# Optimization experiments

Measured on AMD Instinct MI355X. Metric: run time of the kernel, lower is better.

## Reference

```python
import jax, jax.numpy as jnp
import numpy as np

DIM = 64
HID = 64      # hidden_dim
BATCH = 16384


def setup_inputs() -> dict:
    key = jax.random.key(0)
    ks = jax.random.split(key, 11)
    s = 0.05
    x = jax.random.normal(ks[0], (BATCH, DIM), dtype=jnp.float32)
    # network 0: Linear(1,H) -> ReLU -> Linear(H,2)
    w0 = jax.random.normal(ks[1], (1, HID), dtype=jnp.float32) * s
    b0 = jax.random.normal(ks[2], (HID,), dtype=jnp.float32) * s
    v0 = jax.random.normal(ks[3], (HID, 2), dtype=jnp.float32) * s
    c0 = jax.random.normal(ks[4], (2,), dtype=jnp.float32) * s
    # networks 1..DIM-1: Linear(i,H) -> ReLU -> Linear(H,H) -> ReLU -> Linear(H,2)
    # first-layer weights padded to full width DIM; columns >= i are masked out in reference().
    W1 = jax.random.normal(ks[5], (DIM - 1, DIM, HID), dtype=jnp.float32) * s
    B1 = jax.random.normal(ks[6], (DIM - 1, HID), dtype=jnp.float32) * s
    W2 = jax.random.normal(ks[7], (DIM - 1, HID, HID), dtype=jnp.float32) * s
    B2 = jax.random.normal(ks[8], (DIM - 1, HID), dtype=jnp.float32) * s
    W3 = jax.random.normal(ks[9], (DIM - 1, HID, 2), dtype=jnp.float32) * s
    B3 = jax.random.normal(ks[10], (DIM - 1, 2), dtype=jnp.float32) * s
    return {"x": x, "w0": w0, "b0": b0, "v0": v0, "c0": c0,
            "W1": W1, "B1": B1, "W2": W2, "B2": B2, "W3": W3, "B3": B3}


def reference(x, w0, b0, v0, c0, W1, B1, W2, B2, W3, B3):
    B, dim = x.shape
    # mask[i, j] = 1 if j < (i+1): network i+1 sees x[:, :i+1] prefix of width i+1... actually width i+1? No:
    # network index k (k = 1..dim-1) sees x[:, :k]. Row i of the stacks corresponds to k = i+1,
    # so valid input columns are j < i+1.
    mask = (jnp.arange(dim)[None, :] <= jnpp_dummy) if False else (jnp.arange(dim)[None, :] < (jnp.arange(1, dim)[:, None]))
    mask = mask.astype(x.dtype)                      # [dim-1, dim]
    W1m = W1 * mask[:, :, None]                      # zero out padded input columns
    h1 = jax.nn.relu(jnp.einsum('bd,idh->bih', x, W1m) + B1)   # [B, dim-1, H]
    h2 = jax.nn.relu(jnp.einsum('bih,ihg->big', h1, W2) + B2)  # [B, dim-1, H]
    out = jnp.einsum('big,igo->bio', h2, W3) + B3               # [B, dim-1, 2]
    # network 0 receives a constant ones input -> output is constant across the batch
    h0 = jax.nn.relu(w0[0] + b0)                     # [H]
    out0 = h0 @ v0 + c0                              # [2]
    out0 = jnp.broadcast_to(out0[None, None, :], (B, 1, 2))
    full = jnp.concatenate([out0, out], axis=1)      # [B, dim, 2]
    scales = jnp.clip(full[..., 0], -5.0, 5.0)
    translations = full[..., 1]
    return scales, translations

jnp_dummy = None
```

## Files before the change

### kernel.cpp

```cpp
#include <hip/hip_runtime.h>
#include <hip/hip_bf16.h>

#define BATCH 16384

typedef __attribute__((ext_vector_type(8))) short short8;
typedef __attribute__((ext_vector_type(4))) short short4v;
typedef __attribute__((ext_vector_type(2))) short sshort2;
typedef __attribute__((ext_vector_type(8))) unsigned short ushort8;
typedef __attribute__((ext_vector_type(4))) unsigned short ushort4v;
typedef __attribute__((ext_vector_type(4))) float float4v;

#define FR_STRIDE  18944u
#define FR_SIZE    (63u * FR_STRIDE)
#define OFF_A2     8192u
#define OFF_A3     16384u
#define OFF_B1     18432u
#define OFF_B2     18688u
#define XBF_SIZE   2097152u
#define FR_ELEMS   1184

__device__ __forceinline__ unsigned int packbf2(float a, float b) {
#if __has_builtin(__builtin_amdgcn_cvt_pk_bf16_f32)
    typedef __attribute__((ext_vector_type(2))) __bf16 bf2_t;
    union { bf2_t h; unsigned int u; } v;
    v.h = __builtin_amdgcn_cvt_pk_bf16_f32(a, b);
    return v.u;
#else
    union { __hip_bfloat162 h; unsigned int u; } v;
    v.h = __float22bfloat162_rn(make_float2(a, b));
    return v.u;
#endif
}
__device__ __forceinline__ unsigned int relu_pk(unsigned int u) {
#if __has_builtin(__builtin_elementwise_max)
    union { sshort2 s; unsigned int w; } v; v.w = u;
    v.s = __builtin_elementwise_max(v.s, (sshort2)0);
    return v.w;
#else
    unsigned int lo = (u & 0x8000u) ? 0u : (u & 0xFFFFu);
    unsigned int hi = (u & 0x80000000u) ? 0u : (u & 0xFFFF0000u);
    return lo | hi;
#endif
}
__device__ __forceinline__ unsigned int cvt_relu(float a, float b) {
    return relu_pk(packbf2(a, b));
}
__device__ __forceinline__ unsigned short f2bf(float a) {
    union { __hip_bfloat16 h; unsigned short u; } v;
    v.h = __float2bfloat16(a);
    return v.u;
}

__device__ __forceinline__ void gl_lds16(const char* gsrc, char* ldst) {
    __builtin_amdgcn_global_load_lds(
        (const __attribute__((address_space(1))) unsigned int*)gsrc,
        (__attribute__((address_space(3))) unsigned int*)ldst,
        16, 0, 0);
}

__global__ __launch_bounds__(256) void setup_kernel(
    const float* __restrict__ x,
    const float* __restrict__ W1,
    const float* __restrict__ W2,
    const float* __restrict__ W3,
    const float* __restrict__ B1,
    const float* __restrict__ B2,
    char* __restrict__ frag,
    char* __restrict__ xbf)
{
    const int b = blockIdx.x;
    const int t = threadIdx.x;

    if (b >= 63) {
        const int idx = (b - 63) * 256 + t;
        const float* xp = x + (size_t)idx * 16;
        char* dst = xbf + (size_t)idx * 32;
        #pragma unroll
        for (int h = 0; h < 2; ++h) {
            float4v f0 = *(const float4v*)(xp + h * 8);
            float4v f1 = *(const float4v*)(xp + h * 8 + 4);
            union { ushort8 s; unsigned int u[4]; } p;
            p.u[0] = packbf2(f0[0], f0[1]);
            p.u[1] = packbf2(f0[2], f0[3]);
            p.u[2] = packbf2(f1[0], f1[1]);
            p.u[3] = packbf2(f1[2], f1[3]);
            *(ushort8*)(dst + h * 16) = p.s;
        }
        return;
    }

    __shared__ float sW1[4096];
    __shared__ float sW2[4096];

    const int kn   = b;
    const int net  = kn + 1;
    const int lane = t & 63;
    const int grp  = t >> 6;
    const int lq   = lane & 15;
    const int quad = lane >> 4;

    {
        const float4v* s1 = (const float4v*)(W1 + kn * 4096);
        const float4v* s2 = (const float4v*)(W2 + kn * 4096);
        #pragma unroll
        for (int i = 0; i < 4; ++i) {
            ((float4v*)sW1)[i * 256 + t] = s1[i * 256 + t];
            ((float4v*)sW2)[i * 256 + t] = s2[i * 256 + t];
        }
    }
    __syncthreads();

    char* base = frag + (size_t)kn * FR_STRIDE;

    {
        const int h = lq + 16 * grp;
        ushort8 a10, a11;
        #pragma unroll
        for (int j = 0; j < 8; ++j) {
            const int d0 = quad * 8 + j;
            const int d1 = d0 + 32;
            a10[j] = (d0 < net) ? f2bf(sW1[d0 * 64 + h]) : (unsigned short)0;
            a11[j] = (d1 < net) ? f2bf(sW1[d1 * 64 + h]) : (unsigned short)0;
        }
        char* dst = base + grp * 2048 + lane * 32;
        *(ushort8*)(dst)      = a10;
        *(ushort8*)(dst + 16) = a11;
    }

    {
        const int g = lq + 16 * grp;
        #pragma unroll
        for (int p = 0; p < 2; ++p) {
            ushort8 v;
            #pragma unroll
            for (int j = 0; j < 8; ++j) {
                const int h = 32 * p + ((j & 4) << 2) + 4 * quad + (j & 3);
                v[j] = f2bf(sW2[h * 64 + g]);
            }
            *(ushort8*)(base + OFF_A2 + p * 4096 + grp * 1024 + lane * 16) = v;
        }
    }

    if (grp < 2) {
        const int p = grp;
        ushort8 v;
        #pragma unroll
        for (int j = 0; j < 8; ++j) {
            const int gg = 32 * p + ((j & 4) << 2) + 4 * quad + (j & 3);
            v[j] = (lq < 2) ? f2bf(W3[kn * 128 + gg * 2 + lq]) : (unsigned short)0;
        }
        *(ushort8*)(base + OFF_A3 + p * 1024 + lane * 16) = v;
    }

    if (t < 64) {
        *(float*)(base + OFF_B1 + t * 4) = B1[kn * 64 + t];
        *(float*)(base + OFF_B2 + t * 4) = B2[kn * 64 + t];
    }
}

template <bool XBF>
__global__ __launch_bounds__(256, 3) void arnet_main4(
    const float* __restrict__ x,
    const char* __restrict__ xbf,
    const char* __restrict__ frag,
    const float* __restrict__ w0, const float* __restrict__ b0,
    const float* __restrict__ v0, const float* __restrict__ c0,
    const float* __restrict__ B3,
    float* __restrict__ out)
{
    const int bi    = blockIdx.x;
    const int chunk = bi & 63;
    const int gi    = bi >> 6;
    const int start = (gi < 8) ? 6 * gi : 48 + 4 * (gi - 8);
    const int cnt   = (gi < 8) ? 6 : 4;
    const int t     = threadIdx.x;

    const int lane = t & 63;
    const int w    = t >> 6;
    const int lq   = lane & 15;
    const int quad = lane >> 4;

    __shared__ __align__(16) char sFrag[2][FR_STRIDE];
    __shared__ float sOut[2][256][7];

    const int rowbase = chunk * 256 + w * 64;

    short8 xf[4][2];
    #pragma unroll
    for (int tm = 0; tm < 4; ++tm) {
        if (XBF) {
            const char* base = xbf + (size_t)(rowbase + 16 * tm + lq) * 128 + quad * 16;
            xf[tm][0] = *(const short8*)(base);
            xf[tm][1] = *(const short8*)(base + 64);
        } else {
            const float* xr = x + (size_t)(rowbase + 16 * tm + lq) * 64 + quad * 8;
            #pragma unroll
            for (int half = 0; half < 2; ++half) {
                float4v f0 = *(const float4v*)(xr + 32 * half);
                float4v f1 = *(const float4v*)(xr + 32 * half + 4);
                union { short8 s; unsigned int u[4]; } p;
                p.u[0] = packbf2(f0[0], f0[1]);
                p.u[1] = packbf2(f0[2], f0[3]);
                p.u[2] = packbf2(f1[0], f1[1]);
                p.u[3] = packbf2(f1[2], f1[3]);
                xf[tm][half] = p.s;
            }
        }
    }

    auto stage = [&](int net_, char* dstb) {
        const char* src = frag + (size_t)(net_ - 1) * FR_STRIDE;
        #pragma unroll
        for (int i = 0; i < 5; ++i) {
            const int e = i * 256 + t;
            if (e < FR_ELEMS)
                gl_lds16(src + e * 16, dstb + e * 16);
        }
    };

    const int first = (start == 0) ? 1 : 0;
    stage(start + first, sFrag[first & 1]);
    __syncthreads();

    #pragma unroll 1
    for (int idx = 0; idx < cnt; ++idx) {
        const int net = start + idx;

        if (idx + 1 < cnt && idx + 1 > first)
            stage(start + idx + 1, sFrag[(idx + 1) & 1]);

        if (net == 0) {
            float s = 0.f, tr = 0.f;
            #pragma unroll 8
            for (int j = 0; j < 64; ++j) {
                float h = fmaxf(w0[j] + b0[j], 0.f);
                s  += h * v0[2 * j];
                tr += h * v0[2 * j + 1];
            }
            s += c0[0];
            tr += c0[1];
            s = fminf(fmaxf(s, -5.f), 5.f);
            sOut[0][t][0] = s;
            sOut[1][t][0] = tr;
            __syncthreads();
            continue;
        }

        const int kn = net - 1;
        const char* sf  = sFrag[idx & 1];
        const char* pA1 = sf + lane * 32;
        const char* pA2 = sf + OFF_A2 + lane * 16;
        const char* pA3 = sf + OFF_A3 + lane * 16;
        const float* bB1 = (const float*)(sf + OFF_B1);
        const float* bB2 = (const float*)(sf + OFF_B2);

        const bool hiK = (net > 32);
        float4v acc2[4][4];
        #pragma unroll
        for (int p = 0; p < 2; ++p) {
            unsigned int pk[2][2][4];
            #pragma unroll
            for (int s = 0; s < 2; ++s) {
                const int th = 2 * p + s;
                short8 a10 = *(const short8*)(pA1 + th * 2048);
                float4v bias1 = *(const float4v*)(bB1 + quad * 4 + 16 * th);
                if (hiK) {
                    short8 a11 = *(const short8*)(pA1 + th * 2048 + 16);
                    #pragma unroll
                    for (int tm = 0; tm < 4; ++tm) {
                        float4v acc1;
                        acc1 = __builtin_amdgcn_mfma_f32_16x16x32_bf16(a10, xf[tm][0], bias1, 0, 0, 0);
                        acc1 = __builtin_amdgcn_mfma_f32_16x16x32_bf16(a11, xf[tm][1], acc1, 0, 0, 0);
                        pk[s][0][tm] = cvt_relu(acc1[0], acc1[1]);
                        pk[s][1][tm] = cvt_relu(acc1[2], acc1[3]);
                    }
                } else {
                    #pragma unroll
                    for (int tm = 0; tm < 4; ++tm) {
                        float4v acc1;
                        acc1 = __builtin_amdgcn_mfma_f32_16x16x32_bf16(a10, xf[tm][0], bias1, 0, 0, 0);
                        pk[s][0][tm] = cvt_relu(acc1[0], acc1[1]);
                        pk[s][1][tm] = cvt_relu(acc1[2], acc1[3]);
                    }
                }
            }
            #pragma unroll
            for (int tg = 0; tg < 4; ++tg) {
                short8 a2 = *(const short8*)(pA2 + p * 4096 + tg * 1024);
                float4v bias2 = *(const float4v*)(bB2 + quad * 4 + 16 * tg);
                #pragma unroll
                for (int tm = 0; tm < 4; ++tm) {
                    union { short8 s8; unsigned int u[4]; } bb;
                    bb.u[0] = pk[0][0][tm]; bb.u[1] = pk[0][1][tm];
                    bb.u[2] = pk[1][0][tm]; bb.u[3] = pk[1][1][tm];
                    acc2[tg][tm] = __builtin_amdgcn_mfma_f32_16x16x32_bf16(
                        a2, bb.s8, (p == 0) ? bias2 : acc2[tg][tm], 0, 0, 0);
                }
            }
        }

        float4v c3v;
        c3v[0] = B3[kn * 2]; c3v[1] = B3[kn * 2 + 1]; c3v[2] = 0.f; c3v[3] = 0.f;
        float4v acc3[4];
        #pragma unroll
        for (int p = 0; p < 2; ++p) {
            short8 a3 = *(const short8*)(pA3 + p * 1024);
            #pragma unroll
            for (int tm = 0; tm < 4; ++tm) {
                union { short8 s8; unsigned int u[4]; } bb;
                bb.u[0] = cvt_relu(acc2[2 * p][tm][0],     acc2[2 * p][tm][1]);
                bb.u[1] = cvt_relu(acc2[2 * p][tm][2],     acc2[2 * p][tm][3]);
                bb.u[2] = cvt_relu(acc2[2 * p + 1][tm][0], acc2[2 * p + 1][tm][1]);
                bb.u[3] = cvt_relu(acc2[2 * p + 1][tm][2], acc2[2 * p + 1][tm][3]);
                acc3[tm] = __builtin_amdgcn_mfma_f32_16x16x32_bf16(
                    a3, bb.s8, (p == 0) ? c3v : acc3[tm], 0, 0, 0);
            }
        }

        if (quad == 0) {
            #pragma unroll
            for (int tm = 0; tm < 4; ++tm) {
                const int lr = w * 64 + 16 * tm + lq;
                sOut[0][lr][idx] = fminf(fmaxf(acc3[tm][0], -5.f), 5.f);
                sOut[1][lr][idx] = acc3[tm][1];
            }
        }
        __syncthreads();
    }

    {
        const int row = t;
        const size_t grow = (size_t)chunk * 256 + row;
        #pragma unroll
        for (int o = 0; o < 2; ++o) {
            float* dst = out + ((size_t)o * BATCH + grow) * 64 + start;
            #pragma unroll
            for (int c = 0; c < 6; c += 2) {
                if (c < cnt) {
                    float2 v2;
                    v2.x = sOut[o][row][c];
                    v2.y = sOut[o][row][c + 1];
                    *(float2*)(dst + c) = v2;
                }
            }
        }
    }
}

#define WPAD 72
__global__ __launch_bounds__(256) void arnet_fallback(
    const float* __restrict__ x, const float* __restrict__ w0, const float* __restrict__ b0,
    const float* __restrict__ v0, const float* __restrict__ c0,
    const float* __restrict__ W1, const float* __restrict__ B1,
    const float* __restrict__ W2, const float* __restrict__ B2,
    const float* __restrict__ W3, const float* __restrict__ B3,
    float* __restrict__ out)
{
    const int bi = blockIdx.x;
    const int net = bi >> 5;
    const int tile = bi & 31;
    const int t = threadIdx.x;
    if (net == 0) {
        float s = 0.f, tr = 0.f;
        for (int j = 0; j < 64; ++j) {
            float h = fmaxf(w0[j] + b0[j], 0.f);
            s += h * v0[2 * j]; tr += h * v0[2 * j + 1];
        }
        s += c0[0]; tr += c0[1];
        s = fminf(fmaxf(s, -5.f), 5.f);
        const size_t r0 = (size_t)tile * 512;
        out[(r0 + t) * 64] = s; out[(size_t)BATCH * 64 + (r0 + t) * 64] = tr;
        out[(r0 + 256 + t) * 64] = s; out[(size_t)BATCH * 64 + (r0 + 256 + t) * 64] = tr;
        return;
    }
    __shared__ unsigned short sW1T[64 * WPAD];
    __shared__ unsigned short sW2T[64 * WPAD];
    __shared__ unsigned short sW3T[2 * 64];
    __shared__ float sB1[64];
    __shared__ float sB2[64];
    const int kn = net - 1;
    {
        const int hb = (t & 15) * 4, jb = (t >> 4) * 4;
        const float* src1 = W1 + kn * 4096;
        const float* src2 = W2 + kn * 4096;
        float4v a[4], b[4];
        for (int jj = 0; jj < 4; ++jj) {
            a[jj] = *(const float4v*)(src1 + (jb + jj) * 64 + hb);
            if (jb + jj >= net) a[jj] = (float4v)0.f;
            b[jj] = *(const float4v*)(src2 + (jb + jj) * 64 + hb);
        }
        for (int hh = 0; hh < 4; ++hh) {
            ushort4v ra, rb;
            for (int jj = 0; jj < 4; ++jj) { ra[jj] = f2bf(a[jj][hh]); rb[jj] = f2bf(b[jj][hh]); }
            *(ushort4v*)(&sW1T[(hb + hh) * WPAD + jb]) = ra;
            *(ushort4v*)(&sW2T[(hb + hh) * WPAD + jb]) = rb;
        }
    }
    if (t < 64) {
        sW3T[t] = f2bf(W3[kn * 128 + t * 2]);
        sW3T[64 + t] = f2bf(W3[kn * 128 + t * 2 + 1]);
        sB1[t] = B1[kn * 64 + t];
        sB2[t] = B2[kn * 64 + t];
    }
    const float b30 = B3[kn * 2], b31 = B3[kn * 2 + 1];
    __syncthreads();
    const int lane = t & 63, w = t >> 6, lq = lane & 15, quad = lane >> 4;
    for (int pass = 0; pass < 2; ++pass) {
        const int rowbase = tile * 512 + pass * 256 + w * 64;
        short8 xf[4][2];
        for (int tm = 0; tm < 4; ++tm) {
            const float* xr = x + (size_t)(rowbase + 16 * tm + lq) * 64 + quad * 8;
            for (int half = 0; half < 2; ++half) {
                float4v f0 = *(const float4v*)(xr + 32 * half);
                float4v f1 = *(const float4v*)(xr + 32 * half + 4);
                union { short8 s; unsigned int u[4]; } p;
                p.u[0] = packbf2(f0[0], f0[1]); p.u[1] = packbf2(f0[2], f0[3]);
                p.u[2] = packbf2(f1[0], f1[1]); p.u[3] = packbf2(f1[2], f1[3]);
                xf[tm][half] = p.s;
            }
        }
        float4v acc2[4][4];
        for (int tg = 0; tg < 4; ++tg) {
            float4v bias2 = *(const float4v*)(&sB2[quad * 4 + 16 * tg]);
            for (int tm = 0; tm < 4; ++tm) acc2[tg][tm] = bias2;
        }
        for (int th = 0; th < 4; ++th) {
            float4v bias1 = *(const float4v*)(&sB1[quad * 4 + 16 * th]);
            short8 a10 = *(const short8*)(&sW1T[(lq + 16 * th) * WPAD + quad * 8]);
            short8 a11 = *(const short8*)(&sW1T[(lq + 16 * th) * WPAD + quad * 8 + 32]);
            float4v acc1[4];
            for (int tm = 0; tm < 4; ++tm) {
                acc1[tm] = bias1;
                acc1[tm] = __builtin_amdgcn_mfma_f32_16x16x32_bf16(a10, xf[tm][0], acc1[tm], 0, 0, 0);
                acc1[tm] = __builtin_amdgcn_mfma_f32_16x16x32_bf16(a11, xf[tm][1], acc1[tm], 0, 0, 0);
            }
            short4v bf1[4];
            for (int tm = 0; tm < 4; ++tm) {
                union { short4v s; unsigned int u[2]; } pk;
                pk.u[0] = cvt_relu(acc1[tm][0], acc1[tm][1]);
                pk.u[1] = cvt_relu(acc1[tm][2], acc1[tm][3]);
                bf1[tm] = pk.s;
            }
            for (int tg = 0; tg < 4; ++tg) {
                short4v a2 = *(const short4v*)(&sW2T[(lq + 16 * tg) * WPAD + quad * 4 + 16 * th]);
                for (int tm = 0; tm < 4; ++tm)
                    acc2[tg][tm] = __builtin_amdgcn_mfma_f32_16x16x16bf16_1k(a2, bf1[tm], acc2[tg][tm], 0, 0, 0);
            }
        }
        float4v acc3[4];
        for (int tm = 0; tm < 4; ++tm) { acc3[tm][0] = b30; acc3[tm][1] = b31; acc3[tm][2] = 0.f; acc3[tm][3] = 0.f; }
        for (int tg = 0; tg < 4; ++tg) {
            short4v a3 = (short4v)0;
            if (lq < 2) a3 = *(const short4v*)(&sW3T[lq * 64 + quad * 4 + 16 * tg]);
            for (int tm = 0; tm < 4; ++tm) {
                union { short4v s; unsigned int u[2]; } pk;
                pk.u[0] = cvt_relu(acc2[tg][tm][0], acc2[tg][tm][1]);
                pk.u[1] = cvt_relu(acc2[tg][tm][2], acc2[tg][tm][3]);
                acc3[tm] = __builtin_amdgcn_mfma_f32_16x16x16bf16_1k(a3, pk.s, acc3[tm], 0, 0, 0);
            }
        }
        if (quad == 0) {
            for (int tm = 0; tm < 4; ++tm) {
                const size_t r = (size_t)(rowbase + 16 * tm + lq);
                out[r * 64 + net] = fminf(fmaxf(acc3[tm][0], -5.f), 5.f);
                out[(size_t)BATCH * 64 + r * 64 + net] = acc3[tm][1];
            }
        }
    }
}

extern "C" void kernel_launch(void* const* d_in, const int* in_sizes, int n_in,
                              void* d_out, int out_size, void* d_ws, size_t ws_size,
                              hipStream_t stream) {
    const float* x  = (const float*)d_in[0];
    const float* w0 = (const float*)d_in[1];
    const float* b0 = (const float*)d_in[2];
    const float* v0 = (const float*)d_in[3];
    const float* c0 = (const float*)d_in[4];
    const float* W1 = (const float*)d_in[5];
    const float* B1 = (const float*)d_in[6];
    const float* W2 = (const float*)d_in[7];
    const float* B2 = (const float*)d_in[8];
    const float* W3 = (const float*)d_in[9];
    const float* B3 = (const float*)d_in[10];
    float* out = (float*)d_out;
    char* ws = (char*)d_ws;

    const dim3 blk(256);

    if (ws_size >= FR_SIZE + XBF_SIZE) {
        char* xbf = ws + FR_SIZE;
        setup_kernel<<<dim3(63 + 256), blk, 0, stream>>>(x, W1, W2, W3, B1, B2, ws, xbf);
        arnet_main4<true><<<dim3(768), blk, 0, stream>>>(
            x, xbf, ws, w0, b0, v0, c0, B3, out);
    } else if (ws_size >= FR_SIZE) {
        setup_kernel<<<dim3(63), blk, 0, stream>>>(x, W1, W2, W3, B1, B2, ws, nullptr);
        arnet_main4<false><<<dim3(768), blk, 0, stream>>>(
            x, nullptr, ws, w0, b0, v0, c0, B3, out);
    } else {
        arnet_fallback<<<dim3(64 * 32), blk, 0, stream>>>(
            x, w0, b0, v0, c0, W1, B1, W2, B2, W3, B3, out);
    }
}
```

Before: 102.4 us.

## Balance per-block network assignment via pair table and raise MFMA wave priority

```diff
diff --git a/kernel.cpp b/kernel.cpp
--- a/kernel.cpp
+++ b/kernel.cpp
@@ -18,6 +18,12 @@
 #define OFF_B2     18688u
 #define XBF_SIZE   2097152u
 #define FR_ELEMS   1184
+
+__device__ const unsigned char PAIR_TBL[12][3] = {
+    {0, 1, 24}, {2, 3, 25}, {4, 5, 26}, {6, 7, 27},
+    {8, 9, 28}, {10, 11, 29}, {12, 13, 30}, {14, 15, 16},
+    {17, 18, 0}, {19, 20, 0}, {21, 22, 0}, {23, 31, 0}
+};
 
 __device__ __forceinline__ unsigned int packbf2(float a, float b) {
 #if __has_builtin(__builtin_amdgcn_cvt_pk_bf16_f32)
@@ -171,8 +177,8 @@
     const int bi    = blockIdx.x;
     const int chunk = bi & 63;
     const int gi    = bi >> 6;
-    const int start = (gi < 8) ? 6 * gi : 48 + 4 * (gi - 8);
-    const int cnt   = (gi < 8) ? 6 : 4;
+    const int npair = (gi < 8) ? 3 : 2;
+    const int cnt   = 2 * npair;
     const int t     = threadIdx.x;
 
     const int lane = t & 63;
@@ -184,6 +190,10 @@
     __shared__ float sOut[2][256][7];
 
     const int rowbase = chunk * 256 + w * 64;
+
+    auto netof = [&](int i) -> int {
+        return 2 * (int)PAIR_TBL[gi][i >> 1] + (i & 1);
+    };
 
     short8 xf[4][2];
     #pragma unroll
@@ -218,16 +228,16 @@
         }
     };
 
-    const int first = (start == 0) ? 1 : 0;
-    stage(start + first, sFrag[first & 1]);
+    const int first = (gi == 0) ? 1 : 0;
+    stage(netof(first), sFrag[first & 1]);
     __syncthreads();
 
     #pragma unroll 1
     for (int idx = 0; idx < cnt; ++idx) {
-        const int net = start + idx;
+        const int net = netof(idx);
 
         if (idx + 1 < cnt && idx + 1 > first)
-            stage(start + idx + 1, sFrag[(idx + 1) & 1]);
+            stage(netof(idx + 1), sFrag[(idx + 1) & 1]);
 
         if (net == 0) {
             float s = 0.f, tr = 0.f;
@@ -284,6 +294,7 @@
                     }
                 }
             }
+            __builtin_amdgcn_s_setprio(1);
             #pragma unroll
             for (int tg = 0; tg < 4; ++tg) {
                 short8 a2 = *(const short8*)(pA2 + p * 4096 + tg * 1024);
@@ -297,11 +308,13 @@
                         a2, bb.s8, (p == 0) ? bias2 : acc2[tg][tm], 0, 0, 0);
                 }
             }
+            __builtin_amdgcn_s_setprio(0);
         }
 
         float4v c3v;
         c3v[0] = B3[kn * 2]; c3v[1] = B3[kn * 2 + 1]; c3v[2] = 0.f; c3v[3] = 0.f;
         float4v acc3[4];
+        __builtin_amdgcn_s_setprio(1);
         #pragma unroll
         for (int p = 0; p < 2; ++p) {
             short8 a3 = *(const short8*)(pA3 + p * 1024);
@@ -316,6 +329,7 @@
                     a3, bb.s8, (p == 0) ? c3v : acc3[tm], 0, 0, 0);
             }
         }
+        __builtin_amdgcn_s_setprio(0);
 
         if (quad == 0) {
             #pragma unroll
@@ -333,14 +347,14 @@
         const size_t grow = (size_t)chunk * 256 + row;
         #pragma unroll
         for (int o = 0; o < 2; ++o) {
-            float* dst = out + ((size_t)o * BATCH + grow) * 64 + start;
-            #pragma unroll
-            for (int c = 0; c < 6; c += 2) {
-                if (c < cnt) {
+            float* dst = out + ((size_t)o * BATCH + grow) * 64;
+            #pragma unroll
+            for (int j = 0; j < 3; ++j) {
+                if (j < npair) {
                     float2 v2;
-                    v2.x = sOut[o][row][c];
-                    v2.y = sOut[o][row][c + 1];
-                    *(float2*)(dst + c) = v2;
+                    v2.x = sOut[o][row][2 * j];
+                    v2.y = sOut[o][row][2 * j + 1];
+                    *(float2*)(dst + 2 * (int)PAIR_TBL[gi][j]) = v2;
                 }
             }
         }
```

After: 104.5 us. 2.0% more time.
